# Kernel optimization log

Hardware: AMD Instinct MI355X
Metric: run time of the kernel (lower is better)

## Reference

```python
import jax, jax.numpy as jnp
import numpy as np

N = 30000          # mesh vertices
B = 5 * 16         # p_bins * t_bins geodesic patch bins
NEURONS = [16, 64, 64, 32]


def setup_inputs() -> dict:
    key = jax.random.key(0)
    ks = jax.random.split(key, 7)
    x = jax.random.normal(ks[0], (N, NEURONS[0]), dtype=jnp.float32)
    conn = jax.random.randint(ks[1], (N, B), 0, N)  # per-vertex per-bin source index
    s1 = 1.0 / np.sqrt(NEURONS[0])
    W1 = jax.random.uniform(ks[2], (NEURONS[0], NEURONS[1]), minval=-s1, maxval=s1, dtype=jnp.float32)
    s2 = 1.0 / np.sqrt(B * NEURONS[1])
    Wg1 = jax.random.uniform(ks[3], (B, NEURONS[1], NEURONS[2]), minval=-s2, maxval=s2, dtype=jnp.float32)
    b1 = jax.random.uniform(ks[4], (NEURONS[2],), minval=-s2, maxval=s2, dtype=jnp.float32)
    s3 = 1.0 / np.sqrt(B * NEURONS[2])
    Wg2 = jax.random.uniform(ks[5], (B, NEURONS[2], NEURONS[3]), minval=-s3, maxval=s3, dtype=jnp.float32)
    b2 = jax.random.uniform(ks[6], (NEURONS[3],), minval=-s3, maxval=s3, dtype=jnp.float32)
    return {"x": x, "W1": W1, "Wg1": Wg1, "b1": b1, "Wg2": Wg2, "b2": b2, "conn": conn}


def _geodesic(h, conn, Wg, b):
    # gather geodesic patch: [N, B, C_in], then per-bin contraction
    patches = h[conn]                               # irregular gather
    return jnp.einsum("nbi,bio->no", patches, Wg) + b


def reference(x, W1, Wg1, b1, Wg2, b2, conn):
    h = jax.nn.relu(x @ W1)                         # linear_1 (no bias, l_bias=False)
    h = jax.nn.relu(_geodesic(h, conn, Wg1, b1))    # GC_1 + relu
    res = _geodesic(h, conn, Wg2, b2)               # GC_2
    norm = jnp.linalg.norm(res, axis=-1, keepdims=True)
    return res / norm
```

## Files before the change

### kernel.cpp

```cpp
#include <hip/hip_runtime.h>
#include <stdint.h>
#include <stddef.h>


typedef __attribute__((ext_vector_type(8))) short bf16x8;
typedef __attribute__((ext_vector_type(4))) float f32x4;

#define BINS 80
#define SPLITK1 4
#define SPLITK2 8
#define PFD 5

static __device__ __forceinline__ unsigned short f2bf(float f) {
  union { float f; unsigned int u; } c; c.f = f;
  unsigned int u = c.u;
  return (unsigned short)((u + 0x7FFFu + ((u >> 16) & 1u)) >> 16);
}

static __device__ __forceinline__ void wait_vm(int m) {
  if (m >= 10)      asm volatile("s_waitcnt vmcnt(10)");
  else if (m == 8)  asm volatile("s_waitcnt vmcnt(8)");
  else if (m == 6)  asm volatile("s_waitcnt vmcnt(6)");
  else if (m == 4)  asm volatile("s_waitcnt vmcnt(4)");
  else if (m == 2)  asm volatile("s_waitcnt vmcnt(2)");
  else              asm volatile("s_waitcnt vmcnt(0)");
}

__global__ __launch_bounds__(256) void k_lin1(const float* __restrict__ x,
                                              const float* __restrict__ W1,
                                              unsigned short* __restrict__ h1b, int n) {
  __shared__ float w1s[16 * 64];
  int tid = threadIdx.x;
  for (int i = tid; i < 16 * 64; i += 256) w1s[i] = W1[i];
  __syncthreads();
  int v = blockIdx.x * 256 + tid;
  if (v >= n) return;
  const float4* xp = (const float4*)(x + (size_t)v * 16);
  float4 x0 = xp[0], x1 = xp[1], x2 = xp[2], x3 = xp[3];
  float xr[16] = {x0.x, x0.y, x0.z, x0.w, x1.x, x1.y, x1.z, x1.w,
                  x2.x, x2.y, x2.z, x2.w, x3.x, x3.y, x3.z, x3.w};
  float acc[64];
#pragma unroll
  for (int o = 0; o < 64; ++o) acc[o] = 0.f;
#pragma unroll
  for (int i = 0; i < 16; ++i) {
    float xi = xr[i];
#pragma unroll
    for (int o = 0; o < 64; ++o) acc[o] = fmaf(xi, w1s[i * 64 + o], acc[o]);
  }
  unsigned short* hr = h1b + (size_t)v * 64;
#pragma unroll
  for (int o8 = 0; o8 < 8; ++o8) {
    bf16x8 pack;
#pragma unroll
    for (int j = 0; j < 8; ++j) pack[j] = (short)f2bf(fmaxf(acc[o8 * 8 + j], 0.f));
    *(bf16x8*)(hr + o8 * 8) = pack;
  }
}

__global__ __launch_bounds__(256) void k_wimg(const float* __restrict__ Wg,
                                              unsigned char* __restrict__ img,
                                              int O, int total) {
  int t = blockIdx.x * 256 + threadIdx.x;
  if (t >= total) return;
  int j = t & 3;
  int r = t >> 2;
  int o = r % O;
  int r2 = r / O;
  int z = r2 & 1;
  int b = r2 >> 1;
  bf16x8 pack;
#pragma unroll
  for (int tt = 0; tt < 8; ++tt)
    pack[tt] = (short)f2bf(Wg[(size_t)(b * 64 + z * 32 + j * 8 + tt) * O + o]);
  size_t boff = (size_t)b * (O * 128) + z * (O * 64) + o * 64 + ((j + (o >> 1)) & 3) * 16;
  *(bf16x8*)(img + boff) = pack;
}

template <int OT, int BPCT>
__global__ __launch_bounds__(512, 4) void k_geo4(const unsigned short* __restrict__ hin,
                                                 const unsigned char* __restrict__ wimg,
                                                 const int* __restrict__ conn,
                                                 float* __restrict__ part, int n) {
  constexpr int SLAB = OT * 1024;
  constexpr int TOT = BPCT * SLAB;
  constexpr int RR = (TOT + 8191) / 8192;
  __shared__ alignas(16) unsigned char wg_s[TOT];

  const int tid = threadIdx.x;
  const int lane = tid & 63;
  const int wave = tid >> 6;
  const int ln15 = lane & 15;
  const int lq = lane >> 4;
  const int v0 = blockIdx.x * 256;
  const int bin0 = blockIdx.y * BPCT;

  int vv0 = v0 + wave * 32 + ln15;      if (vv0 > n - 1) vv0 = n - 1;
  int vv1 = v0 + wave * 32 + 16 + ln15; if (vv1 > n - 1) vv1 = n - 1;

  auto stage = [&](int ph) {
#pragma unroll
    for (int r = 0; r < RR; ++r) {
      int off = (r * 512 + tid) * 16;
      if (off < TOT) {
        int bin = off / SLAB;
        int within = off & (SLAB - 1);
        __builtin_amdgcn_global_load_lds(
            (const __attribute__((address_space(1))) unsigned int*)(const void*)
                (wimg + (size_t)(bin0 + bin) * (2 * SLAB) + ph * SLAB + within),
            (__attribute__((address_space(3))) unsigned int*)(void*)(wg_s + off),
            16, 0, 0);
      }
    }
  };

  stage(0);

  unsigned int cpk[BPCT];
#pragma unroll
  for (int j = 0; j < BPCT; ++j) {
    int c0 = conn[(size_t)vv0 * BINS + bin0 + j];
    int c1 = conn[(size_t)vv1 * BINS + bin0 + j];
    cpk[j] = ((unsigned)c0 & 0xffffu) | ((unsigned)c1 << 16);
  }
  __builtin_amdgcn_sched_barrier(0);

  int boffs[OT];
#pragma unroll
  for (int ot = 0; ot < OT; ++ot) {
    int o = ot * 16 + ln15;
    boffs[ot] = o * 64 + ((lq + (o >> 1)) & 3) * 16;
  }

  const int koff = lq * 8;

  bf16x8 As[6][2];
  f32x4 acc[2][OT];
#pragma unroll
  for (int mt = 0; mt < 2; ++mt)
#pragma unroll
    for (int ot = 0; ot < OT; ++ot) acc[mt][ot] = (f32x4){0.f, 0.f, 0.f, 0.f};

#define ISSUE(ph, j) do {                                                        \
    int c0_ = (int)(cpk[(j)] & 0xffffu);                                         \
    int c1_ = (int)(cpk[(j)] >> 16);                                             \
    const void* p0_ = (const void*)(hin + (size_t)c0_ * 64 + (ph) * 32 + koff);  \
    const void* p1_ = (const void*)(hin + (size_t)c1_ * 64 + (ph) * 32 + koff);  \
    asm volatile("global_load_dwordx4 %0, %1, off" : "=v"(As[(j) % 6][0]) : "v"(p0_)); \
    asm volatile("global_load_dwordx4 %0, %1, off" : "=v"(As[(j) % 6][1]) : "v"(p1_)); \
  } while (0)

  auto run_phase = [&](int ph) {
#pragma unroll
    for (int b = 0; b < BPCT; ++b) {
      if (b + PFD < BPCT) ISSUE(ph, b + PFD);
      int rem = BPCT - 1 - b;
      wait_vm(2 * (rem > PFD ? PFD : rem));
      __builtin_amdgcn_sched_barrier(0);
      const unsigned char* wb = wg_s + b * SLAB;
#pragma unroll
      for (int ot = 0; ot < OT; ++ot) {
        bf16x8 bf = *(const bf16x8*)(wb + boffs[ot]);
        acc[0][ot] = __builtin_amdgcn_mfma_f32_16x16x32_bf16(As[b % 6][0], bf, acc[0][ot], 0, 0, 0);
        acc[1][ot] = __builtin_amdgcn_mfma_f32_16x16x32_bf16(As[b % 6][1], bf, acc[1][ot], 0, 0, 0);
      }
    }
  };

#pragma unroll
  for (int j = 0; j < PFD; ++j) ISSUE(0, j);
  wait_vm(2 * PFD);
  __builtin_amdgcn_s_barrier();
  __builtin_amdgcn_sched_barrier(0);
  run_phase(0);

  asm volatile("s_waitcnt lgkmcnt(0)" ::: "memory");
  __builtin_amdgcn_s_barrier();
  __builtin_amdgcn_sched_barrier(0);
  stage(1);
#pragma unroll
  for (int j = 0; j < PFD; ++j) ISSUE(1, j);
  wait_vm(2 * PFD);
  __builtin_amdgcn_s_barrier();
  __builtin_amdgcn_sched_barrier(0);
  run_phase(1);
#undef ISSUE

  constexpr int O = OT * 16;
  float* pbase = part + (size_t)blockIdx.y * n * O;
#pragma unroll
  for (int mt = 0; mt < 2; ++mt)
#pragma unroll
    for (int ot = 0; ot < OT; ++ot)
#pragma unroll
      for (int r = 0; r < 4; ++r) {
        int v = v0 + wave * 32 + mt * 16 + lq * 4 + r;
        if (v < n) pbase[(size_t)v * O + ot * 16 + ln15] = acc[mt][ot][r];
      }
}

__global__ __launch_bounds__(256) void k_fin1(const float* __restrict__ part,
                                              const float* __restrict__ bias,
                                              unsigned short* __restrict__ out, int n) {
  int t = blockIdx.x * 256 + threadIdx.x;
  int total = n * 16;
  if (t >= total) return;
  int base = t * 4;
  int o = base & 63;
  size_t stride = (size_t)n * 64;
  const float* p = part + base;
  f32x4 s = *(const f32x4*)(p);
#pragma unroll
  for (int c = 1; c < SPLITK1; ++c) {
    f32x4 q = *(const f32x4*)(p + c * stride);
    s += q;
  }
  const float* b4 = bias + o;
  ushort4 pack;
  pack.x = f2bf(fmaxf(s[0] + b4[0], 0.f));
  pack.y = f2bf(fmaxf(s[1] + b4[1], 0.f));
  pack.z = f2bf(fmaxf(s[2] + b4[2], 0.f));
  pack.w = f2bf(fmaxf(s[3] + b4[3], 0.f));
  *(ushort4*)(out + base) = pack;
}

__global__ __launch_bounds__(256) void k_fin2(const float* __restrict__ part,
                                              const float* __restrict__ bias,
                                              float* __restrict__ out, int n) {
  int v = blockIdx.x * 16 + (threadIdx.x >> 4);
  int o = threadIdx.x & 15;
  if (v >= n) return;
  size_t stride = (size_t)n * 32;
  const float* p = part + (size_t)v * 32 + o;
  float a = 0.f, b = 0.f;
#pragma unroll
  for (int c = 0; c < SPLITK2; ++c) {
    a += p[c * stride];
    b += p[c * stride + 16];
  }
  a += bias[o];
  b += bias[o + 16];
  float ss = a * a + b * b;
  ss += __shfl_xor(ss, 1);
  ss += __shfl_xor(ss, 2);
  ss += __shfl_xor(ss, 4);
  ss += __shfl_xor(ss, 8);
  float inv = 1.0f / sqrtf(ss);
  out[(size_t)v * 32 + o] = a * inv;
  out[(size_t)v * 32 + 16 + o] = b * inv;
}

extern "C" void kernel_launch(void* const* d_in, const int* in_sizes, int n_in,
                              void* d_out, int out_size, void* d_ws, size_t ws_size,
                              hipStream_t stream) {
  const float* x   = (const float*)d_in[0];
  const float* W1  = (const float*)d_in[1];
  const float* Wg1 = (const float*)d_in[2];
  const float* b1  = (const float*)d_in[3];
  const float* Wg2 = (const float*)d_in[4];
  const float* b2  = (const float*)d_in[5];
  const int*  conn = (const int*)d_in[6];
  int n = in_sizes[0] / 16;

  unsigned char* ws = (unsigned char*)d_ws;
  size_t hb = ((size_t)n * 64 * 2 + 255) & ~(size_t)255;
  unsigned short* h1b = (unsigned short*)(ws);
  unsigned short* h2b = (unsigned short*)(ws + hb);
  unsigned char*  w1i = ws + 2 * hb;
  unsigned char*  w2i = ws + 2 * hb + 80 * 8192;
  float* part = (float*)(ws + 2 * hb + 80 * 8192 + 80 * 4096);

  k_wimg<<<(80 * 2 * 64 * 4 + 255) / 256, 256, 0, stream>>>(Wg1, w1i, 64, 80 * 2 * 64 * 4);
  k_wimg<<<(80 * 2 * 32 * 4 + 255) / 256, 256, 0, stream>>>(Wg2, w2i, 32, 80 * 2 * 32 * 4);
  k_lin1<<<(n + 255) / 256, 256, 0, stream>>>(x, W1, h1b, n);

  int vt = (n + 255) / 256;
  k_geo4<4, 20><<<dim3(vt, SPLITK1), 512, 0, stream>>>(h1b, w1i, conn, part, n);
  k_fin1<<<(n * 16 + 255) / 256, 256, 0, stream>>>(part, b1, h2b, n);
  k_geo4<2, 10><<<dim3(vt, SPLITK2), 512, 0, stream>>>(h2b, w2i, conn, part, n);
  k_fin2<<<(n + 15) / 16, 256, 0, stream>>>(part, b2, (float*)d_out, n);
}
```

Baseline: 152.7 us.

## Partition first geodesic gather by source-vertex range for cache locality

The first geodesic conv now also splits over the source-vertex range. Two z-slices each gather only sources in their half of h1, and out-of-range indices are redirected to an appended zero row at index n. This shrinks each slice's gather working set so it fits better in cache. The cost is doubling the layer-1 MFMA work and partial-sum traffic, with a reduction over 8 pieces instead of 4. Layer 2 keeps a single range with 8 bin splits, and h2's zero row is never written, but no redirect happens there so that row is never read.

```diff
diff --git a/kernel.cpp b/kernel.cpp
--- a/kernel.cpp
+++ b/kernel.cpp
@@ -7,8 +7,7 @@
 typedef __attribute__((ext_vector_type(4))) float f32x4;
 
 #define BINS 80
-#define SPLITK1 4
-#define SPLITK2 8
+#define PIECES 8
 #define PFD 5
 
 static __device__ __forceinline__ unsigned short f2bf(float f) {
@@ -34,7 +33,14 @@
   for (int i = tid; i < 16 * 64; i += 256) w1s[i] = W1[i];
   __syncthreads();
   int v = blockIdx.x * 256 + tid;
-  if (v >= n) return;
+  if (v > n) return;
+  unsigned short* hr = h1b + (size_t)v * 64;
+  if (v == n) {
+    bf16x8 z = (bf16x8){0,0,0,0,0,0,0,0};
+#pragma unroll
+    for (int o8 = 0; o8 < 8; ++o8) *(bf16x8*)(hr + o8 * 8) = z;
+    return;
+  }
   const float4* xp = (const float4*)(x + (size_t)v * 16);
   float4 x0 = xp[0], x1 = xp[1], x2 = xp[2], x3 = xp[3];
   float xr[16] = {x0.x, x0.y, x0.z, x0.w, x1.x, x1.y, x1.z, x1.w,
@@ -48,7 +54,6 @@
 #pragma unroll
     for (int o = 0; o < 64; ++o) acc[o] = fmaf(xi, w1s[i * 64 + o], acc[o]);
   }
-  unsigned short* hr = h1b + (size_t)v * 64;
 #pragma unroll
   for (int o8 = 0; o8 < 8; ++o8) {
     bf16x8 pack;
@@ -81,7 +86,7 @@
 __global__ __launch_bounds__(512, 4) void k_geo4(const unsigned short* __restrict__ hin,
                                                  const unsigned char* __restrict__ wimg,
                                                  const int* __restrict__ conn,
-                                                 float* __restrict__ part, int n) {
+                                                 float* __restrict__ part, int n, int hn) {
   constexpr int SLAB = OT * 1024;
   constexpr int TOT = BPCT * SLAB;
   constexpr int RR = (TOT + 8191) / 8192;
@@ -94,6 +99,8 @@
   const int lq = lane >> 4;
   const int v0 = blockIdx.x * 256;
   const int bin0 = blockIdx.y * BPCT;
+  const int lo = blockIdx.z * hn;
+  const unsigned range = (unsigned)((lo + hn > n ? n : lo + hn) - lo);
 
   int vv0 = v0 + wave * 32 + ln15;      if (vv0 > n - 1) vv0 = n - 1;
   int vv1 = v0 + wave * 32 + 16 + ln15; if (vv1 > n - 1) vv1 = n - 1;
@@ -121,8 +128,12 @@
   for (int j = 0; j < BPCT; ++j) {
     int c0 = conn[(size_t)vv0 * BINS + bin0 + j];
     int c1 = conn[(size_t)vv1 * BINS + bin0 + j];
+    if ((unsigned)(c0 - lo) >= range) c0 = n;
+    if ((unsigned)(c1 - lo) >= range) c1 = n;
     cpk[j] = ((unsigned)c0 & 0xffffu) | ((unsigned)c1 << 16);
   }
+#pragma unroll
+  for (int j = 0; j < BPCT; ++j) asm volatile("" :: "v"(cpk[j]));
   __builtin_amdgcn_sched_barrier(0);
 
   int boffs[OT];
@@ -187,7 +198,7 @@
 #undef ISSUE
 
   constexpr int O = OT * 16;
-  float* pbase = part + (size_t)blockIdx.y * n * O;
+  float* pbase = part + (size_t)(blockIdx.z * gridDim.y + blockIdx.y) * n * O;
 #pragma unroll
   for (int mt = 0; mt < 2; ++mt)
 #pragma unroll
@@ -211,7 +222,7 @@
   const float* p = part + base;
   f32x4 s = *(const f32x4*)(p);
 #pragma unroll
-  for (int c = 1; c < SPLITK1; ++c) {
+  for (int c = 1; c < PIECES; ++c) {
     f32x4 q = *(const f32x4*)(p + c * stride);
     s += q;
   }
@@ -234,7 +245,7 @@
   const float* p = part + (size_t)v * 32 + o;
   float a = 0.f, b = 0.f;
 #pragma unroll
-  for (int c = 0; c < SPLITK2; ++c) {
+  for (int c = 0; c < PIECES; ++c) {
     a += p[c * stride];
     b += p[c * stride + 16];
   }
@@ -263,7 +274,7 @@
   int n = in_sizes[0] / 16;
 
   unsigned char* ws = (unsigned char*)d_ws;
-  size_t hb = ((size_t)n * 64 * 2 + 255) & ~(size_t)255;
+  size_t hb = (((size_t)n + 1) * 64 * 2 + 255) & ~(size_t)255;
   unsigned short* h1b = (unsigned short*)(ws);
   unsigned short* h2b = (unsigned short*)(ws + hb);
   unsigned char*  w1i = ws + 2 * hb;
@@ -272,11 +283,11 @@
 
   k_wimg<<<(80 * 2 * 64 * 4 + 255) / 256, 256, 0, stream>>>(Wg1, w1i, 64, 80 * 2 * 64 * 4);
   k_wimg<<<(80 * 2 * 32 * 4 + 255) / 256, 256, 0, stream>>>(Wg2, w2i, 32, 80 * 2 * 32 * 4);
-  k_lin1<<<(n + 255) / 256, 256, 0, stream>>>(x, W1, h1b, n);
+  k_lin1<<<(n + 1 + 255) / 256, 256, 0, stream>>>(x, W1, h1b, n);
 
   int vt = (n + 255) / 256;
-  k_geo4<4, 20><<<dim3(vt, SPLITK1), 512, 0, stream>>>(h1b, w1i, conn, part, n);
+  k_geo4<4, 20><<<dim3(vt, 4, 2), 512, 0, stream>>>(h1b, w1i, conn, part, n, (n + 1) / 2);
   k_fin1<<<(n * 16 + 255) / 256, 256, 0, stream>>>(part, b1, h2b, n);
-  k_geo4<2, 10><<<dim3(vt, SPLITK2), 512, 0, stream>>>(h2b, w2i, conn, part, n);
+  k_geo4<2, 10><<<dim3(vt, 8, 1), 512, 0, stream>>>(h2b, w2i, conn, part, n, n);
   k_fin2<<<(n + 15) / 16, 256, 0, stream>>>(part, b2, (float*)d_out, n);
 }
```

After: 182.5 us. 19.5% more time.
